# Performance work log

Hardware: AMD Instinct MI355X
Metric: run time of the kernel (lower is better)

## Reference

```python
import jax, jax.numpy as jnp
import numpy as np

N = 8192
IN_F = 512
OUT_F = 128
ALPHA = 0.2  # leaky relu negative slope
NEG_BIG = -1e10
RND_SCALE = 1e5


def setup_inputs() -> dict:
    key = jax.random.key(0)
    k1, k2, k3, k4, k5 = jax.random.split(key, 5)
    h = jax.random.normal(k1, (N, IN_F), dtype=jnp.float32)
    adj = jax.random.randint(k2, (N, N), 0, 2, dtype=jnp.int32)
    W = jax.random.normal(k3, (IN_F, OUT_F), dtype=jnp.float32) * 0.05
    a = jax.random.normal(k4, (2 * OUT_F, 1), dtype=jnp.float32) * 0.1
    # rnd in original is 1e5*(rand-0.5); same distribution here
    rnd = RND_SCALE * (jax.random.uniform(k5, (N, OUT_F), dtype=jnp.float32) - 0.5)
    return {"h": h, "adj": adj, "W": W, "a": a, "rnd": rnd}


def reference(h, adj, W, a, rnd):
    Wh = h @ W                              # [N, OUT_F]
    Wh1 = Wh @ a[:OUT_F, :]                 # [N, 1]
    Wh2 = Wh @ a[OUT_F:, :]                 # [N, 1]
    e = jax.nn.leaky_relu(Wh1 + Wh2.T, negative_slope=ALPHA)  # [N, N]
    attention = jnp.where(adj > 0, e, NEG_BIG)
    attention = jax.nn.softmax(attention, axis=1)
    h_prime = attention @ Wh                # [N, OUT_F]
    h_prime = (h_prime + rnd) / RND_SCALE
    return jax.nn.elu(h_prime)
```

## Files before the change

### kernel.cpp

```cpp
#include <hip/hip_runtime.h>

#define N 8192
#define IN_F 512
#define OUT_F 128
#define SPLITK 8
#define KC 1024
#define LOG2E 1.4426950408889634f
#define LN2 0.6931471805599453f

typedef __attribute__((ext_vector_type(4))) float f32x4;
typedef __attribute__((ext_vector_type(8))) short bf16x8;
typedef __attribute__((ext_vector_type(8))) unsigned short u16x8;
typedef __attribute__((ext_vector_type(4))) int i32x4;

__device__ __forceinline__ short f2bf(float f) {
    union { float f; unsigned u; } c; c.f = f;
    unsigned r = c.u + 0x7FFFu + ((c.u >> 16) & 1u);
    return (short)(r >> 16);
}

__device__ __forceinline__ float exp2fast(float x) {
#if __has_builtin(__builtin_amdgcn_exp2f)
    return __builtin_amdgcn_exp2f(x);
#else
    return __expf(x * LN2);
#endif
}

__device__ __forceinline__ void load_lds16(const void* g, void* l) {
    __builtin_amdgcn_global_load_lds((const __attribute__((address_space(1))) unsigned*)g,
                                     (__attribute__((address_space(3))) unsigned*)l,
                                     16, 0, 0);
}

__global__ __launch_bounds__(256) void prep(const float* __restrict__ W,
                                            short* __restrict__ WT) {
    int idx = blockIdx.x * 256 + threadIdx.x;
    int n = idx & (OUT_F - 1);
    int k = idx >> 7;
    WT[(size_t)n * IN_F + k] = f2bf(W[idx]);
}

__global__ __launch_bounds__(256) void gemm_hW(const float* __restrict__ h,
                                               const short* __restrict__ WT,
                                               const float* __restrict__ a,
                                               short* __restrict__ WhT,
                                               float* __restrict__ sOut,
                                               float* __restrict__ tOut) {
    const int tid = threadIdx.x;
    const int wave = tid >> 6, lane = tid & 63;
    const int row16 = lane & 15, kgrp = lane >> 4;
    const int m0 = blockIdx.x * 16;
    const int kbase = wave * 128;

    f32x4 acc[8] = {};
    const float4* hp = (const float4*)(h + (size_t)(m0 + row16) * IN_F + kbase);

#pragma unroll
    for (int kk = 0; kk < 128; kk += 32) {
        float4 u0 = hp[kk / 4 + kgrp * 2];
        float4 u1 = hp[kk / 4 + kgrp * 2 + 1];
        bf16x8 af;
        af[0] = f2bf(u0.x); af[1] = f2bf(u0.y); af[2] = f2bf(u0.z); af[3] = f2bf(u0.w);
        af[4] = f2bf(u1.x); af[5] = f2bf(u1.y); af[6] = f2bf(u1.z); af[7] = f2bf(u1.w);
#pragma unroll
        for (int nt = 0; nt < 8; nt++) {
            bf16x8 bf_ = *(const bf16x8*)(WT + (size_t)(nt * 16 + row16) * IN_F + kbase + kk + kgrp * 8);
            acc[nt] = __builtin_amdgcn_mfma_f32_16x16x32_bf16(af, bf_, acc[nt], 0, 0, 0);
        }
    }

    __shared__ float red[4][16][132];
#pragma unroll
    for (int nt = 0; nt < 8; nt++)
#pragma unroll
        for (int r = 0; r < 4; r++)
            red[wave][kgrp * 4 + r][nt * 16 + row16] = acc[nt][r];
    __syncthreads();

    const int row = tid >> 4, seg = tid & 15;
    float v[8];
#pragma unroll
    for (int e = 0; e < 8; e++) {
        int c = seg * 8 + e;
        v[e] = red[0][row][c] + red[1][row][c] + red[2][row][c] + red[3][row][c];
    }
    float sp = 0.f, tp = 0.f;
#pragma unroll
    for (int e = 0; e < 8; e++) {
        sp += v[e] * a[seg * 8 + e];
        tp += v[e] * a[OUT_F + seg * 8 + e];
    }
    sp += __shfl_xor(sp, 1); tp += __shfl_xor(tp, 1);
    sp += __shfl_xor(sp, 2); tp += __shfl_xor(tp, 2);
    sp += __shfl_xor(sp, 4); tp += __shfl_xor(tp, 4);
    sp += __shfl_xor(sp, 8); tp += __shfl_xor(tp, 8);
    if (seg == 0) {
        sOut[m0 + row] = sp * LOG2E;
        tOut[m0 + row] = tp * LOG2E;
    }
#pragma unroll
    for (int e = 0; e < 8; e++)
        WhT[(size_t)(seg * 8 + e) * N + m0 + row] = f2bf(v[e]);
}

__global__ __launch_bounds__(256, 4) void attn(const int* __restrict__ adj,
                                               const short* __restrict__ WhT,
                                               const float* __restrict__ s,
                                               const float* __restrict__ t,
                                               unsigned short* __restrict__ num,
                                               float* __restrict__ lpart) {
    const int tid = threadIdx.x;
    const int wave = tid >> 6, lane = tid & 63;
    const int row16 = lane & 15, kgrp = lane >> 4;
    const int kb = blockIdx.x & 7;
    const int mb = blockIdx.x >> 3;
    const int m0 = mb * 64 + wave * 16;
    const int m  = m0 + row16;
    const int ks = kb * KC;

    __shared__ short Bs[2][2][128 * 32];
    __shared__ float tl[KC];

    const i32x4* ap = (const i32x4*)(adj + (size_t)m * N + ks);
    const int abase = kgrp * 2;

    i32x4 ab[2][4];
#pragma unroll
    for (int d = 0; d < 2; d++)
#pragma unroll
        for (int hh = 0; hh < 2; hh++)
            ab[0][d * 2 + hh] = __builtin_nontemporal_load(ap + d * 8 + abase + hh);

    for (int i = tid; i < KC; i += 256) tl[i] = t[ks + i];
    const float s_m = s[m];

    auto stageB = [&](int sup, int par) {
        const int k0 = ks + sup * 64;
#pragma unroll
        for (int d = 0; d < 2; d++)
#pragma unroll
            for (int q = 0; q < 2; q++) {
                int nrow = wave * 32 + q * 16 + (lane >> 2);
                const short* g = WhT + (size_t)nrow * N + k0 + d * 32 + (lane & 3) * 8;
                load_lds16(g, &Bs[par][d][(wave * 32 + q * 16) * 32]);
            }
    };

    f32x4 acc[8] = {};
    float lsum = 0.f;

    stageB(0, 0);
    __syncthreads();

    for (int spo = 0; spo < 8; spo++) {
#pragma unroll
        for (int ss = 0; ss < 2; ss++) {
            const int sp = spo * 2 + ss;
            const int par = ss;
            if (sp + 1 < 16) {
#pragma unroll
                for (int d = 0; d < 2; d++)
#pragma unroll
                    for (int hh = 0; hh < 2; hh++)
                        ab[ss ^ 1][d * 2 + hh] =
                            __builtin_nontemporal_load(ap + (sp + 1) * 16 + d * 8 + abase + hh);
                stageB(sp + 1, par ^ 1);
            }
#pragma unroll
            for (int d = 0; d < 2; d++) {
                const int g = sp * 2 + d;
                const i32x4 a0 = ab[ss][d * 2 + 0];
                const i32x4 a1 = ab[ss][d * 2 + 1];

                const float* tp = tl + g * 32 + kgrp * 8;
                float4 tA = *(const float4*)tp;
                float4 tB = *(const float4*)(tp + 4);
                float tv[8] = { tA.x, tA.y, tA.z, tA.w, tB.x, tB.y, tB.z, tB.w };

                bf16x8 bfr[8];
                const short* base = &Bs[par][d][0];
#pragma unroll
                for (int ni = 0; ni < 8; ni++)
                    bfr[ni] = *(const bf16x8*)(base + (ni * 16 + row16) * 32 + kgrp * 8);

                bf16x8 af;
                unsigned* au = (unsigned*)&af;
#pragma unroll
                for (int q = 0; q < 4; q++) {
                    const int e0 = 2 * q, e1 = 2 * q + 1;
                    float x0 = s_m + tv[e0];
                    float x1 = s_m + tv[e1];
                    x0 = fmaxf(x0, 0.2f * x0);
                    x1 = fmaxf(x1, 0.2f * x1);
                    unsigned u0 = __float_as_uint(exp2fast(x0)) & 0xFFFF0000u;
                    unsigned u1 = __float_as_uint(exp2fast(x1)) & 0xFFFF0000u;
                    const int av0 = (e0 < 4) ? a0[e0] : a1[e0 - 4];
                    const int av1 = (e1 < 4) ? a0[e1] : a1[e1 - 4];
                    u0 = av0 > 0 ? u0 : 0u;
                    u1 = av1 > 0 ? u1 : 0u;
                    lsum += __uint_as_float(u0);
                    lsum += __uint_as_float(u1);
                    au[q] = (u0 >> 16) | u1;
                }
#pragma unroll
                for (int ni = 0; ni < 8; ni++)
                    acc[ni] = __builtin_amdgcn_mfma_f32_16x16x32_bf16(af, bfr[ni], acc[ni], 0, 0, 0);
            }
            __syncthreads();
        }
    }

    {
        float v = lsum;
        v += __shfl_xor(v, 16);
        v += __shfl_xor(v, 32);
        if (kgrp == 0) lpart[(size_t)kb * N + m] = v;
    }

    unsigned short* np_ = num + ((size_t)kb * N + m0) * OUT_F;
#pragma unroll
    for (int ni = 0; ni < 8; ni++) {
        int n = ni * 16 + row16;
#pragma unroll
        for (int r = 0; r < 4; r++)
            np_[(size_t)(kgrp * 4 + r) * OUT_F + n] = (unsigned short)f2bf(acc[ni][r]);
    }
}

__global__ __launch_bounds__(256) void finalize(const unsigned short* __restrict__ num,
                                                const float* __restrict__ lpart,
                                                const float* __restrict__ rnd,
                                                float* __restrict__ out) {
    int idx = blockIdx.x * 256 + threadIdx.x;
    int m = idx >> 4;
    int c = (idx & 15) * 8;
    size_t g = (size_t)m * OUT_F + c;

    float nm[8] = {};
#pragma unroll
    for (int bk = 0; bk < SPLITK; bk++) {
        u16x8 v = *(const u16x8*)(num + (size_t)bk * N * OUT_F + g);
#pragma unroll
        for (int e = 0; e < 8; e++) nm[e] += __uint_as_float((unsigned)v[e] << 16);
    }
    float l = 0.f;
#pragma unroll
    for (int bk = 0; bk < SPLITK; bk++) l += lpart[(size_t)bk * N + m];
    float inv = 1.f / fmaxf(l, 1e-30f);

    float4 r0 = *(const float4*)(rnd + g);
    float4 r1 = *(const float4*)(rnd + g + 4);
    float rv[8] = { r0.x, r0.y, r0.z, r0.w, r1.x, r1.y, r1.z, r1.w };
    float ov[8];
#pragma unroll
    for (int e = 0; e < 8; e++) {
        float x = (nm[e] * inv + rv[e]) * 1e-5f;
        ov[e] = x > 0.f ? x : __expf(x) - 1.f;
    }
    *(float4*)(out + g)     = make_float4(ov[0], ov[1], ov[2], ov[3]);
    *(float4*)(out + g + 4) = make_float4(ov[4], ov[5], ov[6], ov[7]);
}

extern "C" void kernel_launch(void* const* d_in, const int* in_sizes, int n_in,
                              void* d_out, int out_size, void* d_ws, size_t ws_size,
                              hipStream_t stream) {
    const float* h   = (const float*)d_in[0];
    const int*   adj = (const int*)d_in[1];
    const float* W   = (const float*)d_in[2];
    const float* a   = (const float*)d_in[3];
    const float* rnd = (const float*)d_in[4];
    float* out = (float*)d_out;

    char* w = (char*)d_ws;
    short* WT    = (short*)(w);
    short* WhT   = (short*)(w + 131072);
    float* sv    = (float*)(w + 2228224);
    float* tv    = (float*)(w + 2260992);
    float* lpart = (float*)(w + 2293760);
    unsigned short* num  = (unsigned short*)(w + 2555904);

    prep    <<<256, 256, 0, stream>>>(W, WT);
    gemm_hW <<<512, 256, 0, stream>>>(h, WT, a, WhT, sv, tv);
    attn    <<<1024, 256, 0, stream>>>(adj, WhT, sv, tv, num, lpart);
    finalize<<<512, 256, 0, stream>>>(num, lpart, rnd, out);
}
```

Baseline: 423.5 us.

## Warp-specialize attn: producer waves pack adjacency into LDS bitmasks

```diff
diff --git a/kernel.cpp b/kernel.cpp
--- a/kernel.cpp
+++ b/kernel.cpp
@@ -104,7 +104,7 @@
         WhT[(size_t)(seg * 8 + e) * N + m0 + row] = f2bf(v[e]);
 }
 
-__global__ __launch_bounds__(256, 4) void attn(const int* __restrict__ adj,
+__global__ __launch_bounds__(512, 4) void attn(const int* __restrict__ adj,
                                                const short* __restrict__ WhT,
                                                const float* __restrict__ s,
                                                const float* __restrict__ t,
@@ -112,66 +112,52 @@
                                                float* __restrict__ lpart) {
     const int tid = threadIdx.x;
     const int wave = tid >> 6, lane = tid & 63;
-    const int row16 = lane & 15, kgrp = lane >> 4;
     const int kb = blockIdx.x & 7;
     const int mb = blockIdx.x >> 3;
-    const int m0 = mb * 64 + wave * 16;
-    const int m  = m0 + row16;
+    const int m0blk = mb * 64;
     const int ks = kb * KC;
 
     __shared__ short Bs[2][2][128 * 32];
     __shared__ float tl[KC];
-
-    const i32x4* ap = (const i32x4*)(adj + (size_t)m * N + ks);
-    const int abase = kgrp * 2;
-
-    i32x4 ab[2][4];
-#pragma unroll
-    for (int d = 0; d < 2; d++)
-#pragma unroll
-        for (int hh = 0; hh < 2; hh++)
-            ab[0][d * 2 + hh] = __builtin_nontemporal_load(ap + d * 8 + abase + hh);
-
-    for (int i = tid; i < KC; i += 256) tl[i] = t[ks + i];
-    const float s_m = s[m];
-
-    auto stageB = [&](int sup, int par) {
-        const int k0 = ks + sup * 64;
-#pragma unroll
-        for (int d = 0; d < 2; d++)
-#pragma unroll
-            for (int q = 0; q < 2; q++) {
-                int nrow = wave * 32 + q * 16 + (lane >> 2);
-                const short* g = WhT + (size_t)nrow * N + k0 + d * 32 + (lane & 3) * 8;
-                load_lds16(g, &Bs[par][d][(wave * 32 + q * 16) * 32]);
-            }
-    };
-
-    f32x4 acc[8] = {};
-    float lsum = 0.f;
-
-    stageB(0, 0);
-    __syncthreads();
-
-    for (int spo = 0; spo < 8; spo++) {
-#pragma unroll
-        for (int ss = 0; ss < 2; ss++) {
-            const int sp = spo * 2 + ss;
-            const int par = ss;
-            if (sp + 1 < 16) {
-#pragma unroll
-                for (int d = 0; d < 2; d++)
-#pragma unroll
-                    for (int hh = 0; hh < 2; hh++)
-                        ab[ss ^ 1][d * 2 + hh] =
-                            __builtin_nontemporal_load(ap + (sp + 1) * 16 + d * 8 + abase + hh);
-                stageB(sp + 1, par ^ 1);
-            }
+    __shared__ unsigned short maskL[4][64 * 4];
+
+    if (wave < 4) {
+        const int row16 = lane & 15, kgrp = lane >> 4;
+        const int m0 = m0blk + wave * 16;
+        const int m = m0 + row16;
+
+        for (int i = tid; i < KC; i += 256) tl[i] = t[ks + i];
+        const float s_m = s[m];
+
+        auto stageB = [&](int sup, int par) {
+            const int k0 = ks + sup * 64;
+#pragma unroll
+            for (int dd = 0; dd < 2; dd++)
+#pragma unroll
+                for (int q = 0; q < 2; q++) {
+                    int nrow = wave * 32 + q * 16 + (lane >> 2);
+                    const short* gg = WhT + (size_t)nrow * N + k0 + dd * 32 + (lane & 3) * 8;
+                    load_lds16(gg, &Bs[par][dd][(wave * 32 + q * 16) * 32]);
+                }
+        };
+
+        f32x4 acc[8] = {};
+        float lsum = 0.f;
+
+        stageB(0, 0);
+        asm volatile("s_waitcnt vmcnt(0) lgkmcnt(0)\n\ts_barrier" ::: "memory");
+
+        for (int sp = 0; sp < 16; sp++) {
+            const int par = sp & 1;
+            if (sp + 1 < 16) stageB(sp + 1, par ^ 1);
+
+            const unsigned long long mk =
+                ((const unsigned long long*)&maskL[sp & 3][0])[wave * 16 + row16];
+
 #pragma unroll
             for (int d = 0; d < 2; d++) {
                 const int g = sp * 2 + d;
-                const i32x4 a0 = ab[ss][d * 2 + 0];
-                const i32x4 a1 = ab[ss][d * 2 + 1];
+                const unsigned mbyte = (unsigned)((mk >> (d * 32 + kgrp * 8)) & 0xFFull);
 
                 const float* tp = tl + g * 32 + kgrp * 8;
                 float4 tA = *(const float4*)tp;
@@ -195,10 +181,8 @@
                     x1 = fmaxf(x1, 0.2f * x1);
                     unsigned u0 = __float_as_uint(exp2fast(x0)) & 0xFFFF0000u;
                     unsigned u1 = __float_as_uint(exp2fast(x1)) & 0xFFFF0000u;
-                    const int av0 = (e0 < 4) ? a0[e0] : a1[e0 - 4];
-                    const int av1 = (e1 < 4) ? a0[e1] : a1[e1 - 4];
-                    u0 = av0 > 0 ? u0 : 0u;
-                    u1 = av1 > 0 ? u1 : 0u;
+                    u0 = ((mbyte >> e0) & 1u) ? u0 : 0u;
+                    u1 = ((mbyte >> e1) & 1u) ? u1 : 0u;
                     lsum += __uint_as_float(u0);
                     lsum += __uint_as_float(u1);
                     au[q] = (u0 >> 16) | u1;
@@ -207,24 +191,57 @@
                 for (int ni = 0; ni < 8; ni++)
                     acc[ni] = __builtin_amdgcn_mfma_f32_16x16x32_bf16(af, bfr[ni], acc[ni], 0, 0, 0);
             }
-            __syncthreads();
-        }
-    }
-
-    {
-        float v = lsum;
-        v += __shfl_xor(v, 16);
-        v += __shfl_xor(v, 32);
-        if (kgrp == 0) lpart[(size_t)kb * N + m] = v;
-    }
-
-    unsigned short* np_ = num + ((size_t)kb * N + m0) * OUT_F;
-#pragma unroll
-    for (int ni = 0; ni < 8; ni++) {
-        int n = ni * 16 + row16;
-#pragma unroll
-        for (int r = 0; r < 4; r++)
-            np_[(size_t)(kgrp * 4 + r) * OUT_F + n] = (unsigned short)f2bf(acc[ni][r]);
+            asm volatile("s_waitcnt vmcnt(0)\n\ts_barrier" ::: "memory");
+        }
+
+        {
+            float v = lsum;
+            v += __shfl_xor(v, 16);
+            v += __shfl_xor(v, 32);
+            if (kgrp == 0) lpart[(size_t)kb * N + m] = v;
+        }
+
+        unsigned short* np_ = num + ((size_t)kb * N + m0) * OUT_F;
+#pragma unroll
+        for (int ni = 0; ni < 8; ni++) {
+            int n = ni * 16 + row16;
+#pragma unroll
+            for (int r = 0; r < 4; r++)
+                np_[(size_t)(kgrp * 4 + r) * OUT_F + n] = (unsigned short)f2bf(acc[ni][r]);
+        }
+    } else {
+        const int pw = wave - 4;
+        const int prow = pw * 16 + (lane >> 2);
+        const int seg = lane & 3;
+        const i32x4* bp4 = (const i32x4*)(adj + (size_t)(m0blk + prow) * N + ks + seg * 16);
+
+        i32x4 pb[2][4];
+        auto ldss = [&](int ssv, int wh) {
+#pragma unroll
+            for (int q = 0; q < 4; q++)
+                pb[wh][q] = __builtin_nontemporal_load(bp4 + ssv * 16 + q);
+        };
+        auto packw = [&](int wh, int slot) {
+            unsigned u = 0;
+#pragma unroll
+            for (int q = 0; q < 4; q++)
+#pragma unroll
+                for (int j = 0; j < 4; j++)
+                    u |= (unsigned)(pb[wh][q][j] > 0) << (q * 4 + j);
+            maskL[slot][prow * 4 + seg] = (unsigned short)u;
+        };
+
+        ldss(0, 0); ldss(1, 1);
+        packw(0, 0); packw(1, 1);
+        ldss(2, 0); ldss(3, 1);
+        asm volatile("s_waitcnt lgkmcnt(0)\n\ts_barrier" ::: "memory");
+
+        for (int sp = 0; sp < 16; sp++) {
+            const int wh = sp & 1;
+            if (sp + 2 < 16) packw(wh, (sp + 2) & 3);
+            if (sp + 4 < 16) ldss(sp + 4, wh);
+            asm volatile("s_waitcnt lgkmcnt(0)\n\ts_barrier" ::: "memory");
+        }
     }
 }
 
@@ -282,6 +299,6 @@
 
     prep    <<<256, 256, 0, stream>>>(W, WT);
     gemm_hW <<<512, 256, 0, stream>>>(h, WT, a, WhT, sv, tv);
-    attn    <<<1024, 256, 0, stream>>>(adj, WhT, sv, tv, num, lpart);
+    attn    <<<1024, 512, 0, stream>>>(adj, WhT, sv, tv, num, lpart);
     finalize<<<512, 256, 0, stream>>>(num, lpart, rnd, out);
 }
```

Result: slower. 443.9 us (+4.8%).
